# Performance work log

Measured on AMD Instinct MI355X. Metric: run time of the kernel, lower is better.

## Reference

```python
import jax, jax.numpy as jnp
import numpy as np

NUM_CLASSES = 256
FEATURE_DIM = 768
BATCH = 128
SIM_BALANCE = 0.7
TIER1 = 50.0
TIER2 = 10.0
TOPK = 5


def _l2norm(x):
    return x / jnp.linalg.norm(x, axis=1, keepdims=True)


def build_edge_weights(class_features, context_features, w1, b1, w2, b2,
                       co_occurrence, instance_counts):
    """Vectorized, faithful translation of VisualFeatureGraph.build_graph."""
    N = class_features.shape[0]
    dt = class_features.dtype
    co = co_occurrence.astype(dt)            # [N,N], diag is 0
    cnt = instance_counts.astype(dt)         # [N]

    vs = _l2norm(class_features) @ _l2norm(class_features).T    # visual_sim [N,N]
    cs = _l2norm(context_features) @ _l2norm(context_features).T  # context_sim
    combined = SIM_BALANCE * vs + (1.0 - SIM_BALANCE) * cs

    # ---- Tier 1: co > TIER1 ----
    # sim_proj(f_i - f_j): exploit linearity of first layer: (f_i-f_j)@W1 = a_i - a_j
    a = class_features @ w1                                    # [N, D/2]
    h = jax.nn.relu(a[:, None, :] - a[None, :, :] + b1)        # [N,N,D/2]
    sim_weight = jax.nn.sigmoid(h @ w2 + b2)[..., 0]           # [N,N]
    ratio = (jnp.minimum(cnt[:, None], cnt[None, :]) /
             jnp.maximum(jnp.maximum(cnt[:, None], cnt[None, :]), 1.0))
    e1 = combined * sim_weight * ratio

    # ---- Tier 2: TIER2 < co <= TIER1 ----
    # shared neighbors k: co[i,k]>T1 and co[j,k]>T1 (k=i,j auto-excluded: diag=0
    # and co[i,j]<=T1 for tier-2 pairs)
    A = (co > TIER1).astype(dt)                                # [N,N]
    M = vs * A
    shared_sum = M @ M.T                                       # sum_k vs[i,k]*vs[j,k]
    shared_cnt = A @ A.T
    avg_sim = shared_sum / jnp.maximum(shared_cnt, 1.0)
    conf = co / TIER1
    e2 = jnp.where(shared_cnt > 0,
                   conf * combined + (1.0 - conf) * avg_sim,
                   conf * combined)

    # ---- Tier 3: co <= TIER2 ----
    # top-5 neighbors per row by co-occurrence among co > TIER2 (diag=0 and
    # co[i,j]<=TIER2 for tier-3 pairs, so i and j are auto-excluded)
    top_vals, top_idx = jax.lax.top_k(co, TOPK)                # [N,K]
    valid = top_vals > TIER2                                   # [N,K]
    ii = top_idx[:, None, :, None]                             # [N,1,K,1]
    jj = top_idx[None, :, None, :]                             # [1,N,1,K]
    co_cross = co[ii, jj]                                      # co[i_neigh, j_neigh] [N,N,K,K]
    vs_cross = vs[ii, jj]
    vs_in = jnp.take_along_axis(vs, top_idx, axis=1)           # vs[i, i_neigh] [N,K]
    mask = valid[:, None, :, None] & valid[None, :, None, :] & (co_cross > 0)
    w = (top_vals[:, None, :, None] * top_vals[None, :, None, :]) / TIER1
    w = jnp.where(mask, w, 0.0)
    sim = vs_in[:, None, :, None] * vs_in[None, :, None, :] * vs_cross
    trans = jnp.sum(w * sim, axis=(2, 3))                      # [N,N]
    tot = jnp.sum(w, axis=(2, 3))
    e3 = jnp.where(tot > 0, trans / jnp.where(tot > 0, tot, 1.0), 0.1 * cs)

    tier1_mask = co > TIER1
    tier2_mask = (co > TIER2) & ~tier1_mask
    E = jnp.where(tier1_mask, e1, jnp.where(tier2_mask, e2, e3))
    E = E * (1.0 - jnp.eye(N, dtype=dt))                       # i==j skipped
    mx = jnp.max(E)
    E = jnp.where(mx > 0, E / jnp.where(mx > 0, mx, 1.0), E)
    return E


def setup_inputs() -> dict:
    key = jax.random.key(0)
    ks = jax.random.split(key, 8)
    N, D, B = NUM_CLASSES, FEATURE_DIM, BATCH
    x = jax.random.normal(ks[0], (B, N, D), dtype=jnp.float32)
    class_features = jax.random.normal(ks[1], (N, D), dtype=jnp.float32) * 0.05
    context_features = jax.random.normal(ks[2], (N, D), dtype=jnp.float32) * 0.05
    w1 = jax.random.normal(ks[3], (D, D // 2), dtype=jnp.float32) * (1.0 / np.sqrt(D))
    b1 = jnp.zeros((D // 2,), dtype=jnp.float32)
    w2 = jax.random.normal(ks[4], (D // 2, 1), dtype=jnp.float32) * (1.0 / np.sqrt(D // 2))
    b2 = jnp.zeros((1,), dtype=jnp.float32)
    co = jax.random.randint(ks[5], (N, N), 0, 121, dtype=jnp.int32)
    co = (co + co.T) // 2                                      # symmetric like update_features
    co = co * (1 - jnp.eye(N, dtype=jnp.int32))                # zero diagonal
    instance_counts = jax.random.randint(ks[6], (N,), 1, 1001, dtype=jnp.int32)
    return {"x": x, "class_features": class_features,
            "context_features": context_features,
            "w1": w1, "b1": b1, "w2": w2, "b2": b2,
            "co_occurrence": co, "instance_counts": instance_counts}


def reference(x, class_features, context_features, w1, b1, w2, b2,
              co_occurrence, instance_counts):
    E = build_edge_weights(class_features, context_features, w1, b1, w2, b2,
                           co_occurrence, instance_counts)
    # torch.bmm(E.expand(B,-1,-1), x) == einsum over shared node dim
    return x + jnp.einsum('ij,bjd->bid', E, x)
```

## Files before the change

### kernel.cpp

```cpp
#include <hip/hip_runtime.h>
#include <hip/hip_bf16.h>
#include <math.h>

#define N 256
#define D 768
#define BATCH 128

typedef float f32x4 __attribute__((ext_vector_type(4)));
typedef short bf16x8 __attribute__((ext_vector_type(8)));

static __device__ __forceinline__ unsigned short f2bf(float f) {
    unsigned int u = __float_as_uint(f);
    u += 0x7fffu + ((u >> 16) & 1u);
    return (unsigned short)(u >> 16);
}
static __device__ __forceinline__ unsigned int pack2bf(float lo, float hi) {
    unsigned int a = __float_as_uint(lo);
    unsigned int b = __float_as_uint(hi);
    a += 0x7fffu + ((a >> 16) & 1u);
    b += 0x7fffu + ((b >> 16) & 1u);
    return (a >> 16) | (b & 0xffff0000u);
}

__global__ void k_norm(const float* __restrict__ cf, const float* __restrict__ ctx,
                       float* __restrict__ vsn, float* __restrict__ csn) {
    int row = blockIdx.x;
    const float* src;
    float* dst;
    if (row < N) { src = cf  + row * D;       dst = vsn + row * D; }
    else         { src = ctx + (row - N) * D; dst = csn + (row - N) * D; }
    int t = threadIdx.x;
    float s = 0.f;
    for (int d = t; d < D; d += 256) { float v = src[d]; s += v * v; }
    __shared__ float red[256];
    red[t] = s; __syncthreads();
    for (int off = 128; off > 0; off >>= 1) {
        if (t < off) red[t] += red[t + off];
        __syncthreads();
    }
    float inv = 1.0f / sqrtf(red[0]);
    for (int d = t; d < D; d += 256) dst[d] = src[d] * inv;
}

__global__ void k_a2(const float* __restrict__ cf, const float* __restrict__ w1,
                     float* __restrict__ a) {
    int bi = blockIdx.x;
    int i0 = (bi / 12) * 32, j0 = (bi % 12) * 32;
    __shared__ float Ci[64][33], Wj[64][33];
    int t = threadIdx.x;
    int tx = t & 15, ty = t >> 4;
    float a00 = 0.f, a01 = 0.f, a10 = 0.f, a11 = 0.f;
    for (int k0 = 0; k0 < 768; k0 += 64) {
        #pragma unroll
        for (int s = 0; s < 8; s++) {
            int idx = s * 256 + t;
            int row = idx >> 6, kc = idx & 63;
            Ci[kc][row] = cf[(i0 + row) * 768 + k0 + kc];
            int kr = idx >> 5, col = idx & 31;
            Wj[kr][col] = w1[(k0 + kr) * 384 + j0 + col];
        }
        __syncthreads();
        #pragma unroll 4
        for (int kk = 0; kk < 64; kk++) {
            float iv0 = Ci[kk][ty * 2], iv1 = Ci[kk][ty * 2 + 1];
            float jv0 = Wj[kk][tx * 2], jv1 = Wj[kk][tx * 2 + 1];
            a00 += iv0 * jv0; a01 += iv0 * jv1;
            a10 += iv1 * jv0; a11 += iv1 * jv1;
        }
        __syncthreads();
    }
    a[(i0 + ty * 2)     * 384 + j0 + tx * 2]     = a00;
    a[(i0 + ty * 2)     * 384 + j0 + tx * 2 + 1] = a01;
    a[(i0 + ty * 2 + 1) * 384 + j0 + tx * 2]     = a10;
    a[(i0 + ty * 2 + 1) * 384 + j0 + tx * 2 + 1] = a11;
}

__global__ void k_gram2(const float* __restrict__ vsn, const float* __restrict__ csn,
                        float* __restrict__ vs, float* __restrict__ cs) {
    int bx = blockIdx.x;
    const float* S = (bx >= 64) ? csn : vsn;
    float* O       = (bx >= 64) ? cs  : vs;
    int bi = bx & 63;
    int i0 = (bi >> 3) * 32, j0 = (bi & 7) * 32;
    __shared__ float Li[64][33], Lj[64][33];
    int t = threadIdx.x;
    int tx = t & 15, ty = t >> 4;
    float a00 = 0.f, a01 = 0.f, a10 = 0.f, a11 = 0.f;
    for (int k0 = 0; k0 < 768; k0 += 64) {
        #pragma unroll
        for (int s = 0; s < 8; s++) {
            int idx = s * 256 + t;
            int row = idx >> 6, kc = idx & 63;
            Li[kc][row] = S[(i0 + row) * 768 + k0 + kc];
            Lj[kc][row] = S[(j0 + row) * 768 + k0 + kc];
        }
        __syncthreads();
        #pragma unroll 4
        for (int kk = 0; kk < 64; kk++) {
            float iv0 = Li[kk][ty * 2], iv1 = Li[kk][ty * 2 + 1];
            float jv0 = Lj[kk][tx * 2], jv1 = Lj[kk][tx * 2 + 1];
            a00 += iv0 * jv0; a01 += iv0 * jv1;
            a10 += iv1 * jv0; a11 += iv1 * jv1;
        }
        __syncthreads();
    }
    O[(i0 + ty * 2)     * 256 + j0 + tx * 2]     = a00;
    O[(i0 + ty * 2)     * 256 + j0 + tx * 2 + 1] = a01;
    O[(i0 + ty * 2 + 1) * 256 + j0 + tx * 2]     = a10;
    O[(i0 + ty * 2 + 1) * 256 + j0 + tx * 2 + 1] = a11;
}

__global__ __launch_bounds__(256) void k_e1t(
    const float* __restrict__ a, const float* __restrict__ b1,
    const float* __restrict__ w2, const float* __restrict__ b2,
    const float* __restrict__ vs, const float* __restrict__ cs,
    const int* __restrict__ ic, float* __restrict__ e1) {
    int i0 = (blockIdx.x >> 4) * 16, j0 = (blockIdx.x & 15) * 16;
    __shared__ float ai[16][388], ajm[16][388];
    __shared__ float sw2[384];
    int t = threadIdx.x;
    for (int idx = t; idx < 16 * 96; idx += 256) {
        int r = idx / 96, c = (idx % 96) * 4;
        *(float4*)&ai[r][c] = *(const float4*)(a + (i0 + r) * 384 + c);
        float4 u  = *(const float4*)(a + (j0 + r) * 384 + c);
        float4 bb = *(const float4*)(b1 + c);
        u.x -= bb.x; u.y -= bb.y; u.z -= bb.z; u.w -= bb.w;
        *(float4*)&ajm[r][c] = u;
    }
    for (int k = t; k < 384; k += 256) sw2[k] = w2[k];
    __syncthreads();
    int tx = t & 15, ty = t >> 4;
    float s = 0.f;
    #pragma unroll 4
    for (int k4 = 0; k4 < 96; k4++) {
        float4 xv = *(const float4*)&ai[ty][k4 * 4];
        float4 yv = *(const float4*)&ajm[tx][k4 * 4];
        float4 wv = *(const float4*)&sw2[k4 * 4];
        s += fmaxf(xv.x - yv.x, 0.f) * wv.x;
        s += fmaxf(xv.y - yv.y, 0.f) * wv.y;
        s += fmaxf(xv.z - yv.z, 0.f) * wv.z;
        s += fmaxf(xv.w - yv.w, 0.f) * wv.w;
    }
    int i = i0 + ty, j = j0 + tx;
    float sig = 1.0f / (1.0f + expf(-(s + b2[0])));
    float comb = 0.7f * vs[i * 256 + j] + 0.3f * cs[i * 256 + j];
    float ci = (float)ic[i], cj = (float)ic[j];
    float mn = fminf(ci, cj), mx = fmaxf(ci, cj);
    float ratio = mn / fmaxf(mx, 1.0f);
    e1[i * 256 + j] = comb * sig * ratio;
}

__global__ void k_shared2(const int* __restrict__ co, const float* __restrict__ vs,
                          float* __restrict__ ss, float* __restrict__ sc) {
    int bi = blockIdx.x;
    int i0 = (bi >> 3) * 32, j0 = (bi & 7) * 32;
    __shared__ float Mi[64][33], Ai[64][33], Mj[64][33], Aj[64][33];
    int t = threadIdx.x;
    int tx = t & 15, ty = t >> 4;
    float s00=0.f,s01=0.f,s10=0.f,s11=0.f;
    float c00=0.f,c01=0.f,c10=0.f,c11=0.f;
    for (int k0 = 0; k0 < 256; k0 += 64) {
        #pragma unroll
        for (int s = 0; s < 8; s++) {
            int idx = s * 256 + t;
            int row = idx >> 6, kc = idx & 63;
            int ci = co[(i0 + row) * 256 + k0 + kc];
            float aa = ci > 50 ? 1.f : 0.f;
            Ai[kc][row] = aa;
            Mi[kc][row] = aa * vs[(i0 + row) * 256 + k0 + kc];
            int cj = co[(j0 + row) * 256 + k0 + kc];
            float ab = cj > 50 ? 1.f : 0.f;
            Aj[kc][row] = ab;
            Mj[kc][row] = ab * vs[(j0 + row) * 256 + k0 + kc];
        }
        __syncthreads();
        #pragma unroll 4
        for (int kk = 0; kk < 64; kk++) {
            float mi0 = Mi[kk][ty*2], mi1 = Mi[kk][ty*2+1];
            float ai0 = Ai[kk][ty*2], ai1 = Ai[kk][ty*2+1];
            float mj0 = Mj[kk][tx*2], mj1 = Mj[kk][tx*2+1];
            float aj0 = Aj[kk][tx*2], aj1 = Aj[kk][tx*2+1];
            s00 += mi0*mj0; s01 += mi0*mj1; s10 += mi1*mj0; s11 += mi1*mj1;
            c00 += ai0*aj0; c01 += ai0*aj1; c10 += ai1*aj0; c11 += ai1*aj1;
        }
        __syncthreads();
    }
    ss[(i0+ty*2)  *256 + j0+tx*2]   = s00; ss[(i0+ty*2)  *256 + j0+tx*2+1] = s01;
    ss[(i0+ty*2+1)*256 + j0+tx*2]   = s10; ss[(i0+ty*2+1)*256 + j0+tx*2+1] = s11;
    sc[(i0+ty*2)  *256 + j0+tx*2]   = c00; sc[(i0+ty*2)  *256 + j0+tx*2+1] = c01;
    sc[(i0+ty*2+1)*256 + j0+tx*2]   = c10; sc[(i0+ty*2+1)*256 + j0+tx*2+1] = c11;
}

__global__ void k_topk2(const int* __restrict__ co, float* __restrict__ topv,
                        int* __restrict__ topi) {
    int t = threadIdx.x;
    int lane = t & 63;
    int row = blockIdx.x * 4 + (t >> 6);
    int4 v4 = *(const int4*)(co + row * 256 + lane * 4);
    int key[4];
    key[0] = v4.x * 256 + (255 - (lane * 4 + 0));
    key[1] = v4.y * 256 + (255 - (lane * 4 + 1));
    key[2] = v4.z * 256 + (255 - (lane * 4 + 2));
    key[3] = v4.w * 256 + (255 - (lane * 4 + 3));
    for (int r = 0; r < 5; r++) {
        int best = key[0];
        #pragma unroll
        for (int e = 1; e < 4; e++) best = max(best, key[e]);
        #pragma unroll
        for (int off = 32; off > 0; off >>= 1) best = max(best, __shfl_xor(best, off, 64));
        int kidx = 255 - (best & 255);
        int val = best >> 8;
        if (lane == 0) { topv[row * 5 + r] = (float)val; topi[row * 5 + r] = kidx; }
        if ((kidx >> 2) == lane) key[kidx & 3] = -1;
    }
}

__global__ void k_assemble(const int* __restrict__ co, const float* __restrict__ vs,
                           const float* __restrict__ cs, const float* __restrict__ e1,
                           const float* __restrict__ ss, const float* __restrict__ sc,
                           const float* __restrict__ topv, const int* __restrict__ topi,
                           float* __restrict__ E, float* __restrict__ partials) {
    int i = blockIdx.x, j = threadIdx.x;
    int cij = co[i * 256 + j];
    float e;
    if (i == j) {
        e = 0.f;
    } else if (cij > 50) {
        e = e1[i * 256 + j];
    } else if (cij > 10) {
        float conf = (float)cij / 50.0f;
        float comb = 0.7f * vs[i * 256 + j] + 0.3f * cs[i * 256 + j];
        float cnt = sc[i * 256 + j];
        float avg = ss[i * 256 + j] / fmaxf(cnt, 1.f);
        e = (cnt > 0.f) ? conf * comb + (1.f - conf) * avg : conf * comb;
    } else {
        float tvi[5], tvj[5]; int tii[5], tij[5];
        #pragma unroll
        for (int k = 0; k < 5; k++) {
            tvi[k] = topv[i * 5 + k]; tii[k] = topi[i * 5 + k];
            tvj[k] = topv[j * 5 + k]; tij[k] = topi[j * 5 + k];
        }
        float trans = 0.f, tot = 0.f;
        #pragma unroll
        for (int k = 0; k < 5; k++) {
            if (!(tvi[k] > 10.f)) continue;
            float vin_i = vs[i * 256 + tii[k]];
            #pragma unroll
            for (int l = 0; l < 5; l++) {
                if (!(tvj[l] > 10.f)) continue;
                int cc = co[tii[k] * 256 + tij[l]];
                if (cc <= 0) continue;
                float w = tvi[k] * tvj[l] / 50.f;
                float sim = vin_i * vs[j * 256 + tij[l]] * vs[tii[k] * 256 + tij[l]];
                trans += w * sim; tot += w;
            }
        }
        e = (tot > 0.f) ? trans / tot : 0.1f * cs[i * 256 + j];
    }
    E[i * 256 + j] = e;
    __shared__ float red[256];
    red[j] = e; __syncthreads();
    for (int off = 128; off > 0; off >>= 1) {
        if (j < off) red[j] = fmaxf(red[j], red[j + off]);
        __syncthreads();
    }
    if (j == 0) partials[i] = red[0];
}

__global__ void k_ep(const float* __restrict__ E, const float* __restrict__ partials,
                     unsigned short* __restrict__ Ep) {
    __shared__ float red[256];
    int t = threadIdx.x;
    red[t] = partials[t]; __syncthreads();
    for (int off = 128; off > 0; off >>= 1) {
        if (t < off) red[t] = fmaxf(red[t], red[t + off]);
        __syncthreads();
    }
    float mx = red[0];
    float s = (mx > 0.f) ? 1.0f / mx : 1.0f;
    int base = (blockIdx.x * 256 + t) * 4;
    float4 e4 = *(const float4*)(E + base);
    float ev[4] = {e4.x, e4.y, e4.z, e4.w};
    unsigned short o[4];
    #pragma unroll
    for (int q = 0; q < 4; q++) {
        int g = base + q;
        float v = s * ev[q] + (((g >> 8) == (g & 255)) ? 1.0f : 0.0f);
        o[q] = f2bf(v);
    }
    uint2 w;
    w.x = (unsigned int)o[0] | ((unsigned int)o[1] << 16);
    w.y = (unsigned int)o[2] | ((unsigned int)o[3] << 16);
    *(uint2*)(Ep + base) = w;
}

#define PEP 264
#define PXT 40
__global__ __launch_bounds__(256, 1) void k_einsum_mfma(
    const unsigned short* __restrict__ Ep, const float* __restrict__ x,
    float* __restrict__ out) {
    extern __shared__ unsigned short smem[];
    unsigned short* eplds = smem;
    unsigned short* xt    = smem + 256 * PEP;
    int t = threadIdx.x;
    int b = blockIdx.y;
    int d0 = blockIdx.x * 128;

    #pragma unroll
    for (int it = 0; it < 32; it++) {
        int c = it * 256 + t;
        uint4 v = *(const uint4*)(Ep + (size_t)c * 8);
        *(uint4*)&eplds[(c >> 5) * PEP + (c & 31) * 8] = v;
    }

    int dcol = t & 127;
    int kp = (t >> 7) * 2;
    const float* xb = x + ((size_t)b * 256) * 768 + d0 + dcol;

    int lane = t & 63;
    int lq = lane >> 4, l15 = lane & 15;
    int i0w = (t >> 6) * 64;

    f32x4 acc[4][8];
    #pragma unroll
    for (int gm = 0; gm < 4; gm++)
        #pragma unroll
        for (int gn = 0; gn < 8; gn++)
            #pragma unroll
            for (int e = 0; e < 4; e++) acc[gm][gn][e] = 0.f;

    float r0[8], r1[8];
    #pragma unroll
    for (int s = 0; s < 8; s++) {
        int k = kp + 4 * s;
        r0[s] = xb[k * 768];
        r1[s] = xb[(k + 1) * 768];
    }

    for (int kt = 0; kt < 8; kt++) {
        #pragma unroll
        for (int s = 0; s < 8; s++) {
            int k = kp + 4 * s;
            *(unsigned int*)&xt[dcol * PXT + k] = pack2bf(r0[s], r1[s]);
        }
        __syncthreads();
        if (kt < 7) {
            const float* xn = xb + (kt + 1) * 32 * 768;
            #pragma unroll
            for (int s = 0; s < 8; s++) {
                int k = kp + 4 * s;
                r0[s] = xn[k * 768];
                r1[s] = xn[(k + 1) * 768];
            }
        }
        int kg = kt * 32 + lq * 8;
        bf16x8 av[4], bv[8];
        #pragma unroll
        for (int g = 0; g < 4; g++)
            av[g] = *(const bf16x8*)&eplds[(i0w + g * 16 + l15) * PEP + kg];
        #pragma unroll
        for (int g = 0; g < 8; g++)
            bv[g] = *(const bf16x8*)&xt[(g * 16 + l15) * PXT + lq * 8];
        #pragma unroll
        for (int gm = 0; gm < 4; gm++)
            #pragma unroll
            for (int gn = 0; gn < 8; gn++)
                acc[gm][gn] = __builtin_amdgcn_mfma_f32_16x16x32_bf16(
                    av[gm], bv[gn], acc[gm][gn], 0, 0, 0);
        __syncthreads();
    }

    float* ob = out + ((size_t)b * 256) * 768 + d0;
    #pragma unroll
    for (int gm = 0; gm < 4; gm++) {
        #pragma unroll
        for (int gn = 0; gn < 8; gn++) {
            #pragma unroll
            for (int r = 0; r < 4; r++) {
                int i = i0w + gm * 16 + lq * 4 + r;
                int d = gn * 16 + l15;
                ob[(size_t)i * 768 + d] = acc[gm][gn][r];
            }
        }
    }
}

extern "C" void kernel_launch(void* const* d_in, const int* in_sizes, int n_in,
                              void* d_out, int out_size, void* d_ws, size_t ws_size,
                              hipStream_t stream) {
    const float* x   = (const float*)d_in[0];
    const float* cf  = (const float*)d_in[1];
    const float* ctx = (const float*)d_in[2];
    const float* w1  = (const float*)d_in[3];
    const float* b1  = (const float*)d_in[4];
    const float* w2  = (const float*)d_in[5];
    const float* b2  = (const float*)d_in[6];
    const int*   co  = (const int*)d_in[7];
    const int*   ic  = (const int*)d_in[8];
    float* out = (float*)d_out;

    float* ws   = (float*)d_ws;
    float* vsn  = ws;
    float* csn  = vsn + 196608;
    float* a    = csn + 196608;
    float* vs   = a + 98304;
    float* cs   = vs + 65536;
    float* e1   = cs + 65536;
    float* ss   = e1 + 65536;
    float* sc   = ss + 65536;
    float* E    = sc + 65536;
    float* topv = E + 65536;
    int*   topi = (int*)(topv + 1280);
    float* partials = (float*)(topi + 1280);
    unsigned short* Ep = (unsigned short*)(partials + 256);

    k_norm<<<512, 256, 0, stream>>>(cf, ctx, vsn, csn);
    k_a2<<<96, 256, 0, stream>>>(cf, w1, a);
    k_gram2<<<128, 256, 0, stream>>>(vsn, csn, vs, cs);
    k_e1t<<<256, 256, 0, stream>>>(a, b1, w2, b2, vs, cs, ic, e1);
    k_shared2<<<64, 256, 0, stream>>>(co, vs, ss, sc);
    k_topk2<<<64, 256, 0, stream>>>(co, topv, topi);
    k_assemble<<<256, 256, 0, stream>>>(co, vs, cs, e1, ss, sc, topv, topi, E, partials);
    k_ep<<<64, 256, 0, stream>>>(E, partials, Ep);
    size_t lds_bytes = (size_t)(256 * PEP + 128 * PXT) * sizeof(unsigned short);
    k_einsum_mfma<<<dim3(6, BATCH), 256, lds_bytes, stream>>>(Ep, x, out);
}
```

Baseline: 287.5 us.

## Merge independent pre-stage kernels into two block-specialized launches and fold normalization into Gram

Six small kernels are collapsed into two launches whose blocks branch by index. The first runs the w1 projection, top-k and Gram matrices side by side, and the second runs the tier-1 MLP weights next to the shared-neighbor products. L2 normalization no longer writes normalized copies; each Gram block computes row norms itself and scales its dot products at the end. This removes four kernel launches, the idle gaps between them and the normalized-feature round trip through memory. In exchange the norm work is repeated per tile and blocks of very different cost share one grid.

```diff
diff --git a/kernel.cpp b/kernel.cpp
--- a/kernel.cpp
+++ b/kernel.cpp
@@ -22,196 +22,199 @@
     return (a >> 16) | (b & 0xffff0000u);
 }
 
-__global__ void k_norm(const float* __restrict__ cf, const float* __restrict__ ctx,
-                       float* __restrict__ vsn, float* __restrict__ csn) {
-    int row = blockIdx.x;
-    const float* src;
-    float* dst;
-    if (row < N) { src = cf  + row * D;       dst = vsn + row * D; }
-    else         { src = ctx + (row - N) * D; dst = csn + (row - N) * D; }
+__global__ void k_stage1(const float* __restrict__ cf, const float* __restrict__ ctx,
+                         const float* __restrict__ w1, float* __restrict__ a,
+                         const int* __restrict__ co, float* __restrict__ topv,
+                         int* __restrict__ topi,
+                         float* __restrict__ vs, float* __restrict__ cs) {
+    __shared__ float sm[2 * 64 * 33];
+    __shared__ float nsum[64][5];
+    __shared__ float invn[64];
+    int bx = blockIdx.x;
     int t = threadIdx.x;
-    float s = 0.f;
-    for (int d = t; d < D; d += 256) { float v = src[d]; s += v * v; }
-    __shared__ float red[256];
-    red[t] = s; __syncthreads();
-    for (int off = 128; off > 0; off >>= 1) {
-        if (t < off) red[t] += red[t + off];
-        __syncthreads();
-    }
-    float inv = 1.0f / sqrtf(red[0]);
-    for (int d = t; d < D; d += 256) dst[d] = src[d] * inv;
-}
-
-__global__ void k_a2(const float* __restrict__ cf, const float* __restrict__ w1,
-                     float* __restrict__ a) {
-    int bi = blockIdx.x;
-    int i0 = (bi / 12) * 32, j0 = (bi % 12) * 32;
-    __shared__ float Ci[64][33], Wj[64][33];
+    if (bx < 96) {
+        int bi = bx;
+        int i0 = (bi / 12) * 32, j0 = (bi % 12) * 32;
+        float (*Ci)[33] = (float(*)[33])sm;
+        float (*Wj)[33] = (float(*)[33])(sm + 64 * 33);
+        int tx = t & 15, ty = t >> 4;
+        float a00 = 0.f, a01 = 0.f, a10 = 0.f, a11 = 0.f;
+        for (int k0 = 0; k0 < 768; k0 += 64) {
+            #pragma unroll
+            for (int s = 0; s < 8; s++) {
+                int idx = s * 256 + t;
+                int row = idx >> 6, kc = idx & 63;
+                Ci[kc][row] = cf[(i0 + row) * 768 + k0 + kc];
+                int kr = idx >> 5, col = idx & 31;
+                Wj[kr][col] = w1[(k0 + kr) * 384 + j0 + col];
+            }
+            __syncthreads();
+            #pragma unroll 4
+            for (int kk = 0; kk < 64; kk++) {
+                float iv0 = Ci[kk][ty * 2], iv1 = Ci[kk][ty * 2 + 1];
+                float jv0 = Wj[kk][tx * 2], jv1 = Wj[kk][tx * 2 + 1];
+                a00 += iv0 * jv0; a01 += iv0 * jv1;
+                a10 += iv1 * jv0; a11 += iv1 * jv1;
+            }
+            __syncthreads();
+        }
+        a[(i0 + ty * 2)     * 384 + j0 + tx * 2]     = a00;
+        a[(i0 + ty * 2)     * 384 + j0 + tx * 2 + 1] = a01;
+        a[(i0 + ty * 2 + 1) * 384 + j0 + tx * 2]     = a10;
+        a[(i0 + ty * 2 + 1) * 384 + j0 + tx * 2 + 1] = a11;
+    } else if (bx < 160) {
+        int lane = t & 63;
+        int row = (bx - 96) * 4 + (t >> 6);
+        int4 v4 = *(const int4*)(co + row * 256 + lane * 4);
+        int k0 = v4.x * 256 + (255 - (lane * 4 + 0));
+        int k1 = v4.y * 256 + (255 - (lane * 4 + 1));
+        int k2 = v4.z * 256 + (255 - (lane * 4 + 2));
+        int k3 = v4.w * 256 + (255 - (lane * 4 + 3));
+        for (int r = 0; r < 5; r++) {
+            int best = max(max(k0, k1), max(k2, k3));
+            #pragma unroll
+            for (int off = 32; off > 0; off >>= 1) best = max(best, __shfl_xor(best, off, 64));
+            int kidx = 255 - (best & 255);
+            int val = best >> 8;
+            if (lane == 0) { topv[row * 5 + r] = (float)val; topi[row * 5 + r] = kidx; }
+            if ((kidx >> 2) == lane) {
+                int sel = kidx & 3;
+                k0 = (sel == 0) ? -1 : k0;
+                k1 = (sel == 1) ? -1 : k1;
+                k2 = (sel == 2) ? -1 : k2;
+                k3 = (sel == 3) ? -1 : k3;
+            }
+        }
+    } else {
+        int bx2 = bx - 160;
+        const float* S = (bx2 >= 64) ? ctx : cf;
+        float* O       = (bx2 >= 64) ? cs  : vs;
+        int bi = bx2 & 63;
+        int i0 = (bi >> 3) * 32, j0 = (bi & 7) * 32;
+        {
+            int r = t >> 2, p = t & 3;
+            const float* Srow = S + (size_t)((r < 32) ? (i0 + r) : (j0 + r - 32)) * 768;
+            float sq = 0.f;
+            for (int j = 0; j < 192; j++) { float v = Srow[p + 4 * j]; sq += v * v; }
+            nsum[r][p] = sq;
+        }
+        __syncthreads();
+        if (t < 64) invn[t] = 1.0f / sqrtf(nsum[t][0] + nsum[t][1] + nsum[t][2] + nsum[t][3]);
+        __syncthreads();
+        float (*Li)[33] = (float(*)[33])sm;
+        float (*Lj)[33] = (float(*)[33])(sm + 64 * 33);
+        int tx = t & 15, ty = t >> 4;
+        float a00 = 0.f, a01 = 0.f, a10 = 0.f, a11 = 0.f;
+        for (int k0 = 0; k0 < 768; k0 += 64) {
+            #pragma unroll
+            for (int s = 0; s < 8; s++) {
+                int idx = s * 256 + t;
+                int row = idx >> 6, kc = idx & 63;
+                Li[kc][row] = S[(i0 + row) * 768 + k0 + kc];
+                Lj[kc][row] = S[(j0 + row) * 768 + k0 + kc];
+            }
+            __syncthreads();
+            #pragma unroll 4
+            for (int kk = 0; kk < 64; kk++) {
+                float iv0 = Li[kk][ty * 2], iv1 = Li[kk][ty * 2 + 1];
+                float jv0 = Lj[kk][tx * 2], jv1 = Lj[kk][tx * 2 + 1];
+                a00 += iv0 * jv0; a01 += iv0 * jv1;
+                a10 += iv1 * jv0; a11 += iv1 * jv1;
+            }
+            __syncthreads();
+        }
+        float ni0 = invn[ty * 2], ni1 = invn[ty * 2 + 1];
+        float nj0 = invn[32 + tx * 2], nj1 = invn[32 + tx * 2 + 1];
+        O[(i0 + ty * 2)     * 256 + j0 + tx * 2]     = a00 * ni0 * nj0;
+        O[(i0 + ty * 2)     * 256 + j0 + tx * 2 + 1] = a01 * ni0 * nj1;
+        O[(i0 + ty * 2 + 1) * 256 + j0 + tx * 2]     = a10 * ni1 * nj0;
+        O[(i0 + ty * 2 + 1) * 256 + j0 + tx * 2 + 1] = a11 * ni1 * nj1;
+    }
+}
+
+__global__ void k_stage3(const float* __restrict__ a, const float* __restrict__ b1,
+                         const float* __restrict__ w2, const float* __restrict__ b2,
+                         const float* __restrict__ vs, const float* __restrict__ cs,
+                         const int* __restrict__ ic, float* __restrict__ e1,
+                         const int* __restrict__ co, float* __restrict__ ss,
+                         float* __restrict__ sc) {
+    __shared__ float sm[12800];
+    int bx = blockIdx.x;
     int t = threadIdx.x;
-    int tx = t & 15, ty = t >> 4;
-    float a00 = 0.f, a01 = 0.f, a10 = 0.f, a11 = 0.f;
-    for (int k0 = 0; k0 < 768; k0 += 64) {
-        #pragma unroll
-        for (int s = 0; s < 8; s++) {
-            int idx = s * 256 + t;
-            int row = idx >> 6, kc = idx & 63;
-            Ci[kc][row] = cf[(i0 + row) * 768 + k0 + kc];
-            int kr = idx >> 5, col = idx & 31;
-            Wj[kr][col] = w1[(k0 + kr) * 384 + j0 + col];
-        }
-        __syncthreads();
+    if (bx < 256) {
+        int i0 = (bx >> 4) * 16, j0 = (bx & 15) * 16;
+        float (*ai)[388]  = (float(*)[388])sm;
+        float (*ajm)[388] = (float(*)[388])(sm + 16 * 388);
+        float* sw2 = sm + 2 * 16 * 388;
+        for (int idx = t; idx < 16 * 96; idx += 256) {
+            int r = idx / 96, c = (idx % 96) * 4;
+            *(float4*)&ai[r][c] = *(const float4*)(a + (i0 + r) * 384 + c);
+            float4 u  = *(const float4*)(a + (j0 + r) * 384 + c);
+            float4 bb = *(const float4*)(b1 + c);
+            u.x -= bb.x; u.y -= bb.y; u.z -= bb.z; u.w -= bb.w;
+            *(float4*)&ajm[r][c] = u;
+        }
+        for (int k = t; k < 384; k += 256) sw2[k] = w2[k];
+        __syncthreads();
+        int tx = t & 15, ty = t >> 4;
+        float s = 0.f;
         #pragma unroll 4
-        for (int kk = 0; kk < 64; kk++) {
-            float iv0 = Ci[kk][ty * 2], iv1 = Ci[kk][ty * 2 + 1];
-            float jv0 = Wj[kk][tx * 2], jv1 = Wj[kk][tx * 2 + 1];
-            a00 += iv0 * jv0; a01 += iv0 * jv1;
-            a10 += iv1 * jv0; a11 += iv1 * jv1;
-        }
-        __syncthreads();
-    }
-    a[(i0 + ty * 2)     * 384 + j0 + tx * 2]     = a00;
-    a[(i0 + ty * 2)     * 384 + j0 + tx * 2 + 1] = a01;
-    a[(i0 + ty * 2 + 1) * 384 + j0 + tx * 2]     = a10;
-    a[(i0 + ty * 2 + 1) * 384 + j0 + tx * 2 + 1] = a11;
-}
-
-__global__ void k_gram2(const float* __restrict__ vsn, const float* __restrict__ csn,
-                        float* __restrict__ vs, float* __restrict__ cs) {
-    int bx = blockIdx.x;
-    const float* S = (bx >= 64) ? csn : vsn;
-    float* O       = (bx >= 64) ? cs  : vs;
-    int bi = bx & 63;
-    int i0 = (bi >> 3) * 32, j0 = (bi & 7) * 32;
-    __shared__ float Li[64][33], Lj[64][33];
-    int t = threadIdx.x;
-    int tx = t & 15, ty = t >> 4;
-    float a00 = 0.f, a01 = 0.f, a10 = 0.f, a11 = 0.f;
-    for (int k0 = 0; k0 < 768; k0 += 64) {
-        #pragma unroll
-        for (int s = 0; s < 8; s++) {
-            int idx = s * 256 + t;
-            int row = idx >> 6, kc = idx & 63;
-            Li[kc][row] = S[(i0 + row) * 768 + k0 + kc];
-            Lj[kc][row] = S[(j0 + row) * 768 + k0 + kc];
-        }
-        __syncthreads();
-        #pragma unroll 4
-        for (int kk = 0; kk < 64; kk++) {
-            float iv0 = Li[kk][ty * 2], iv1 = Li[kk][ty * 2 + 1];
-            float jv0 = Lj[kk][tx * 2], jv1 = Lj[kk][tx * 2 + 1];
-            a00 += iv0 * jv0; a01 += iv0 * jv1;
-            a10 += iv1 * jv0; a11 += iv1 * jv1;
-        }
-        __syncthreads();
-    }
-    O[(i0 + ty * 2)     * 256 + j0 + tx * 2]     = a00;
-    O[(i0 + ty * 2)     * 256 + j0 + tx * 2 + 1] = a01;
-    O[(i0 + ty * 2 + 1) * 256 + j0 + tx * 2]     = a10;
-    O[(i0 + ty * 2 + 1) * 256 + j0 + tx * 2 + 1] = a11;
-}
-
-__global__ __launch_bounds__(256) void k_e1t(
-    const float* __restrict__ a, const float* __restrict__ b1,
-    const float* __restrict__ w2, const float* __restrict__ b2,
-    const float* __restrict__ vs, const float* __restrict__ cs,
-    const int* __restrict__ ic, float* __restrict__ e1) {
-    int i0 = (blockIdx.x >> 4) * 16, j0 = (blockIdx.x & 15) * 16;
-    __shared__ float ai[16][388], ajm[16][388];
-    __shared__ float sw2[384];
-    int t = threadIdx.x;
-    for (int idx = t; idx < 16 * 96; idx += 256) {
-        int r = idx / 96, c = (idx % 96) * 4;
-        *(float4*)&ai[r][c] = *(const float4*)(a + (i0 + r) * 384 + c);
-        float4 u  = *(const float4*)(a + (j0 + r) * 384 + c);
-        float4 bb = *(const float4*)(b1 + c);
-        u.x -= bb.x; u.y -= bb.y; u.z -= bb.z; u.w -= bb.w;
-        *(float4*)&ajm[r][c] = u;
-    }
-    for (int k = t; k < 384; k += 256) sw2[k] = w2[k];
-    __syncthreads();
-    int tx = t & 15, ty = t >> 4;
-    float s = 0.f;
-    #pragma unroll 4
-    for (int k4 = 0; k4 < 96; k4++) {
-        float4 xv = *(const float4*)&ai[ty][k4 * 4];
-        float4 yv = *(const float4*)&ajm[tx][k4 * 4];
-        float4 wv = *(const float4*)&sw2[k4 * 4];
-        s += fmaxf(xv.x - yv.x, 0.f) * wv.x;
-        s += fmaxf(xv.y - yv.y, 0.f) * wv.y;
-        s += fmaxf(xv.z - yv.z, 0.f) * wv.z;
-        s += fmaxf(xv.w - yv.w, 0.f) * wv.w;
-    }
-    int i = i0 + ty, j = j0 + tx;
-    float sig = 1.0f / (1.0f + expf(-(s + b2[0])));
-    float comb = 0.7f * vs[i * 256 + j] + 0.3f * cs[i * 256 + j];
-    float ci = (float)ic[i], cj = (float)ic[j];
-    float mn = fminf(ci, cj), mx = fmaxf(ci, cj);
-    float ratio = mn / fmaxf(mx, 1.0f);
-    e1[i * 256 + j] = comb * sig * ratio;
-}
-
-__global__ void k_shared2(const int* __restrict__ co, const float* __restrict__ vs,
-                          float* __restrict__ ss, float* __restrict__ sc) {
-    int bi = blockIdx.x;
-    int i0 = (bi >> 3) * 32, j0 = (bi & 7) * 32;
-    __shared__ float Mi[64][33], Ai[64][33], Mj[64][33], Aj[64][33];
-    int t = threadIdx.x;
-    int tx = t & 15, ty = t >> 4;
-    float s00=0.f,s01=0.f,s10=0.f,s11=0.f;
-    float c00=0.f,c01=0.f,c10=0.f,c11=0.f;
-    for (int k0 = 0; k0 < 256; k0 += 64) {
-        #pragma unroll
-        for (int s = 0; s < 8; s++) {
-            int idx = s * 256 + t;
-            int row = idx >> 6, kc = idx & 63;
-            int ci = co[(i0 + row) * 256 + k0 + kc];
-            float aa = ci > 50 ? 1.f : 0.f;
-            Ai[kc][row] = aa;
-            Mi[kc][row] = aa * vs[(i0 + row) * 256 + k0 + kc];
-            int cj = co[(j0 + row) * 256 + k0 + kc];
-            float ab = cj > 50 ? 1.f : 0.f;
-            Aj[kc][row] = ab;
-            Mj[kc][row] = ab * vs[(j0 + row) * 256 + k0 + kc];
-        }
-        __syncthreads();
-        #pragma unroll 4
-        for (int kk = 0; kk < 64; kk++) {
-            float mi0 = Mi[kk][ty*2], mi1 = Mi[kk][ty*2+1];
-            float ai0 = Ai[kk][ty*2], ai1 = Ai[kk][ty*2+1];
-            float mj0 = Mj[kk][tx*2], mj1 = Mj[kk][tx*2+1];
-            float aj0 = Aj[kk][tx*2], aj1 = Aj[kk][tx*2+1];
-            s00 += mi0*mj0; s01 += mi0*mj1; s10 += mi1*mj0; s11 += mi1*mj1;
-            c00 += ai0*aj0; c01 += ai0*aj1; c10 += ai1*aj0; c11 += ai1*aj1;
-        }
-        __syncthreads();
-    }
-    ss[(i0+ty*2)  *256 + j0+tx*2]   = s00; ss[(i0+ty*2)  *256 + j0+tx*2+1] = s01;
-    ss[(i0+ty*2+1)*256 + j0+tx*2]   = s10; ss[(i0+ty*2+1)*256 + j0+tx*2+1] = s11;
-    sc[(i0+ty*2)  *256 + j0+tx*2]   = c00; sc[(i0+ty*2)  *256 + j0+tx*2+1] = c01;
-    sc[(i0+ty*2+1)*256 + j0+tx*2]   = c10; sc[(i0+ty*2+1)*256 + j0+tx*2+1] = c11;
-}
-
-__global__ void k_topk2(const int* __restrict__ co, float* __restrict__ topv,
-                        int* __restrict__ topi) {
-    int t = threadIdx.x;
-    int lane = t & 63;
-    int row = blockIdx.x * 4 + (t >> 6);
-    int4 v4 = *(const int4*)(co + row * 256 + lane * 4);
-    int key[4];
-    key[0] = v4.x * 256 + (255 - (lane * 4 + 0));
-    key[1] = v4.y * 256 + (255 - (lane * 4 + 1));
-    key[2] = v4.z * 256 + (255 - (lane * 4 + 2));
-    key[3] = v4.w * 256 + (255 - (lane * 4 + 3));
-    for (int r = 0; r < 5; r++) {
-        int best = key[0];
-        #pragma unroll
-        for (int e = 1; e < 4; e++) best = max(best, key[e]);
-        #pragma unroll
-        for (int off = 32; off > 0; off >>= 1) best = max(best, __shfl_xor(best, off, 64));
-        int kidx = 255 - (best & 255);
-        int val = best >> 8;
-        if (lane == 0) { topv[row * 5 + r] = (float)val; topi[row * 5 + r] = kidx; }
-        if ((kidx >> 2) == lane) key[kidx & 3] = -1;
+        for (int k4 = 0; k4 < 96; k4++) {
+            float4 xv = *(const float4*)&ai[ty][k4 * 4];
+            float4 yv = *(const float4*)&ajm[tx][k4 * 4];
+            float4 wv = *(const float4*)&sw2[k4 * 4];
+            s += fmaxf(xv.x - yv.x, 0.f) * wv.x;
+            s += fmaxf(xv.y - yv.y, 0.f) * wv.y;
+            s += fmaxf(xv.z - yv.z, 0.f) * wv.z;
+            s += fmaxf(xv.w - yv.w, 0.f) * wv.w;
+        }
+        int i = i0 + ty, j = j0 + tx;
+        float sig = 1.0f / (1.0f + expf(-(s + b2[0])));
+        float comb = 0.7f * vs[i * 256 + j] + 0.3f * cs[i * 256 + j];
+        float ci = (float)ic[i], cj = (float)ic[j];
+        float mn = fminf(ci, cj), mx = fmaxf(ci, cj);
+        float ratio = mn / fmaxf(mx, 1.0f);
+        e1[i * 256 + j] = comb * sig * ratio;
+    } else {
+        int bi = bx - 256;
+        int i0 = (bi >> 3) * 32, j0 = (bi & 7) * 32;
+        float (*Mi)[33] = (float(*)[33])sm;
+        float (*Ai)[33] = (float(*)[33])(sm + 2112);
+        float (*Mj)[33] = (float(*)[33])(sm + 4224);
+        float (*Aj)[33] = (float(*)[33])(sm + 6336);
+        int tx = t & 15, ty = t >> 4;
+        float s00=0.f,s01=0.f,s10=0.f,s11=0.f;
+        float c00=0.f,c01=0.f,c10=0.f,c11=0.f;
+        for (int k0 = 0; k0 < 256; k0 += 64) {
+            #pragma unroll
+            for (int s = 0; s < 8; s++) {
+                int idx = s * 256 + t;
+                int row = idx >> 6, kc = idx & 63;
+                int civ = co[(i0 + row) * 256 + k0 + kc];
+                float aa = civ > 50 ? 1.f : 0.f;
+                Ai[kc][row] = aa;
+                Mi[kc][row] = aa * vs[(i0 + row) * 256 + k0 + kc];
+                int cjv = co[(j0 + row) * 256 + k0 + kc];
+                float ab = cjv > 50 ? 1.f : 0.f;
+                Aj[kc][row] = ab;
+                Mj[kc][row] = ab * vs[(j0 + row) * 256 + k0 + kc];
+            }
+            __syncthreads();
+            #pragma unroll 4
+            for (int kk = 0; kk < 64; kk++) {
+                float mi0 = Mi[kk][ty*2], mi1 = Mi[kk][ty*2+1];
+                float ai0 = Ai[kk][ty*2], ai1 = Ai[kk][ty*2+1];
+                float mj0 = Mj[kk][tx*2], mj1 = Mj[kk][tx*2+1];
+                float aj0 = Aj[kk][tx*2], aj1 = Aj[kk][tx*2+1];
+                s00 += mi0*mj0; s01 += mi0*mj1; s10 += mi1*mj0; s11 += mi1*mj1;
+                c00 += ai0*aj0; c01 += ai0*aj1; c10 += ai1*aj0; c11 += ai1*aj1;
+            }
+            __syncthreads();
+        }
+        ss[(i0+ty*2)  *256 + j0+tx*2]   = s00; ss[(i0+ty*2)  *256 + j0+tx*2+1] = s01;
+        ss[(i0+ty*2+1)*256 + j0+tx*2]   = s10; ss[(i0+ty*2+1)*256 + j0+tx*2+1] = s11;
+        sc[(i0+ty*2)  *256 + j0+tx*2]   = c00; sc[(i0+ty*2)  *256 + j0+tx*2+1] = c01;
+        sc[(i0+ty*2+1)*256 + j0+tx*2]   = c10; sc[(i0+ty*2+1)*256 + j0+tx*2+1] = c11;
     }
 }
 
@@ -414,12 +417,8 @@
     float* partials = (float*)(topi + 1280);
     unsigned short* Ep = (unsigned short*)(partials + 256);
 
-    k_norm<<<512, 256, 0, stream>>>(cf, ctx, vsn, csn);
-    k_a2<<<96, 256, 0, stream>>>(cf, w1, a);
-    k_gram2<<<128, 256, 0, stream>>>(vsn, csn, vs, cs);
-    k_e1t<<<256, 256, 0, stream>>>(a, b1, w2, b2, vs, cs, ic, e1);
-    k_shared2<<<64, 256, 0, stream>>>(co, vs, ss, sc);
-    k_topk2<<<64, 256, 0, stream>>>(co, topv, topi);
+    k_stage1<<<288, 256, 0, stream>>>(cf, ctx, w1, a, co, topv, topi, vs, cs);
+    k_stage3<<<320, 256, 0, stream>>>(a, b1, w2, b2, vs, cs, ic, e1, co, ss, sc);
     k_assemble<<<256, 256, 0, stream>>>(co, vs, cs, e1, ss, sc, topv, topi, E, partials);
     k_ep<<<64, 256, 0, stream>>>(E, partials, Ep);
     size_t lds_bytes = (size_t)(256 * PEP + 128 * PXT) * sizeof(unsigned short);
```

Result: faster. 258.8 us (-10.0%).
